# Optimization experiments

Hardware: AMD Instinct MI355X
Metric: run time of the kernel (lower is better)

The kernel has to match this reference:

```python
import jax, jax.numpy as jnp
import numpy as np

VOCAB, EMB, UNITS = 2000, 64, 512
B, T = 64, 128

def lstm(x_emb, Wx, Wh, b, h0, c0):
    """Keras LSTM: gates order (i, f, g, o), sigmoid recurrent activation, tanh activation.
    x_emb: [B, T, EMB]. Returns (H [B,T,U], h [B,U], c [B,U])."""
    # Precompute input contribution for all timesteps (one big GEMM)
    xz = jnp.einsum('bte,eu->btu', x_emb, Wx) + b  # [B, T, 4U]

    def step(carry, xz_t):
        h, c = carry
        z = xz_t + h @ Wh  # [B, 4U]
        i, f, g, o = jnp.split(z, 4, axis=-1)
        i = jax.nn.sigmoid(i)
        f = jax.nn.sigmoid(f)
        g = jnp.tanh(g)
        o = jax.nn.sigmoid(o)
        c = f * c + i * g
        h = o * jnp.tanh(c)
        return (h, c), h

    (h, c), H = jax.lax.scan(step, (h0, c0), jnp.swapaxes(xz, 0, 1))
    return jnp.swapaxes(H, 0, 1), h, c


def setup_inputs() -> dict:
    key = jax.random.key(0)
    ks = jax.random.split(key, 10)
    s = 0.05
    return {
        'x': jax.random.randint(ks[0], (B, T), 0, VOCAB),
        'y': jax.random.randint(ks[1], (B, T), 0, VOCAB),
        'enc_emb': jax.random.normal(ks[2], (VOCAB, EMB), jnp.float32) * s,
        'enc_Wx': jax.random.normal(ks[3], (EMB, 4 * UNITS), jnp.float32) * s,
        'enc_Wh': jax.random.normal(ks[4], (UNITS, 4 * UNITS), jnp.float32) * s,
        'enc_b': jnp.zeros((4 * UNITS,), jnp.float32),
        'dec_emb': jax.random.normal(ks[5], (VOCAB, EMB), jnp.float32) * s,
        'dec_Wx': jax.random.normal(ks[6], (EMB, 4 * UNITS), jnp.float32) * s,
        'dec_Wh': jax.random.normal(ks[7], (UNITS, 4 * UNITS), jnp.float32) * s,
        'dec_b': jnp.zeros((4 * UNITS,), jnp.float32),
        'dense_W': jax.random.normal(ks[8], (2 * UNITS, VOCAB), jnp.float32) * s,
        'dense_b': jnp.zeros((VOCAB,), jnp.float32),
    }


def reference(x, y, enc_emb, enc_Wx, enc_Wh, enc_b,
              dec_emb, dec_Wx, dec_Wh, dec_b, dense_W, dense_b):
    z0 = jnp.zeros((x.shape[0], UNITS), jnp.float32)
    # Encoder
    H, h, c = lstm(enc_emb[x], enc_Wx, enc_Wh, enc_b, z0, z0)  # H: [B,T,U]
    # Decoder LSTM
    s0 = h
    S, h2, c2 = lstm(dec_emb[y], dec_Wx, dec_Wh, dec_b, h, c)  # S: [B,T,U]
    # Shifted states as attention queries (teacher forcing, Luong dot-attention)
    S_ = jnp.concatenate([s0[:, None, :], S[:, :-1, :]], axis=1)  # [B,T,U]
    scores = jnp.einsum('bqu,bku->bqk', S_, H)  # [B,T,T]
    A = jnp.einsum('bqk,bku->bqu', jax.nn.softmax(scores, axis=-1), H)
    yo = jnp.concatenate([S, A], axis=-1)  # [B,T,2U]
    return jax.nn.softmax(yo @ dense_W + dense_b, axis=-1)  # [B,T,VOCAB]
```

## Files before the change

### kernel.cpp

```cpp
#include <hip/hip_runtime.h>
#include <math.h>

#define NB 64
#define NT 128
#define NE 64
#define NU 512
#define NG 2048
#define NV 2000
#define BU (NB*NU)
#define GRID_LSTM 256
#define KTOT 576
#define HS 584
#define WSTRIDE 584
#define SMEM_BYTES (64*WSTRIDE*2 + 16*HS*2 + 2*8*64*4)

#define ASSC 129
#define APB  136
#define OFF_SSC 0
#define OFF_PB  66048
#define OFF_ASM 100864
#define OFF_BSM 111104
#define SMEM_ATT 121344

typedef __attribute__((ext_vector_type(8))) short bf16x8;
typedef __attribute__((ext_vector_type(4))) float f32x4;
typedef __attribute__((ext_vector_type(8))) unsigned short u16x8;

__device__ __forceinline__ unsigned short f2bf(float x) {
    unsigned int u = __float_as_uint(x);
    u += 0x7FFFu + ((u >> 16) & 1u);
    return (unsigned short)(u >> 16);
}
__device__ __forceinline__ float fsigmoid(float x) {
    return __builtin_amdgcn_rcpf(1.f + __expf(-x));
}
__device__ __forceinline__ float ftanh(float x) {
    return 1.f - 2.f * __builtin_amdgcn_rcpf(__expf(2.f * x) + 1.f);
}

__global__ __launch_bounds__(512, 1)
void lstm2_coop(const int* __restrict__ xids, const int* __restrict__ yids,
                const unsigned short* __restrict__ embb_e,
                const unsigned short* __restrict__ embb_d,
                const unsigned short* __restrict__ WhT_e,
                const unsigned short* __restrict__ WhT_d,
                const float* __restrict__ enc_b, const float* __restrict__ dec_b,
                float* __restrict__ Hbuf, float* __restrict__ Sbuf,
                float* __restrict__ hping, float* __restrict__ hfin,
                unsigned short* __restrict__ yo,
                unsigned int* __restrict__ flags)
{
    extern __shared__ char smem[];
    unsigned short* whb  = (unsigned short*)smem;
    unsigned short* hlds = (unsigned short*)(smem + 64 * WSTRIDE * 2);
    float* zbuf = (float*)(smem + 64 * WSTRIDE * 2 + 16 * HS * 2);

    const int tid  = threadIdx.x;
    const int wv   = tid >> 6;
    const int cl   = tid & 63;
    const int bk   = blockIdx.x;
    const int rg   = bk & 7;
    const int cgi  = bk >> 3;
    const int brow0 = rg * 8;
    const int u0    = cgi * 16;

    const int bl  = tid >> 4;
    const int uug = tid & 15;
    float creg = 0.f;
    float b4[4] = {0.f, 0.f, 0.f, 0.f};
    if (tid < 128) {
#pragma unroll
        for (int g = 0; g < 4; ++g) b4[g] = enc_b[g * 512 + u0 + uug];
    }

    {
        const int cp = tid >> 3, ch = tid & 7;
        const int cg = (cp >> 4) * 512 + u0 + (cp & 15);
        const uint4* src = reinterpret_cast<const uint4*>(WhT_e + (size_t)cg * KTOT + ch * 72);
        uint4* dst = reinterpret_cast<uint4*>(whb + cp * WSTRIDE + ch * 72);
#pragma unroll
        for (int i = 0; i < 9; ++i) dst[i] = src[i];
    }

    const int col = wv * 64 + cl;
#pragma unroll
    for (int b = 0; b < 8; ++b) hlds[b * HS + col] = 0;
    for (int i = tid; i < 8 * HS; i += 512) hlds[8 * HS + i] = 0;
    {
        const int idb = xids[(brow0 + wv) * NT + 0];
        hlds[wv * HS + 512 + cl] = embb_e[(size_t)idb * NE + cl];
    }
    unsigned int* fl = flags + rg * 64;

    for (int T = 0; T < 2 * NT; ++T) {
        const int t = T & (NT - 1);
        float* Ho = (T < NT) ? Hbuf : Sbuf;
        __syncthreads();

        {
            const int g = wv & 3, half = wv >> 2;
            const int rr = cl & 15, kh = cl >> 4;
            f32x4 acc = {0.f, 0.f, 0.f, 0.f};
            const unsigned short* arow = hlds + rr * HS;
            const unsigned short* brow = whb + (g * 16 + rr) * WSTRIDE;
#pragma unroll
            for (int kt = 0; kt < 9; ++kt) {
                const int kb = (half * 9 + kt) * 32 + kh * 8;
                bf16x8 af = *reinterpret_cast<const bf16x8*>(arow + kb);
                bf16x8 bf = *reinterpret_cast<const bf16x8*>(brow + kb);
                acc = __builtin_amdgcn_mfma_f32_16x16x32_bf16(af, bf, acc, 0, 0, 0);
            }
            if (cl < 32) {
#pragma unroll
                for (int reg = 0; reg < 4; ++reg)
                    zbuf[half * 512 + (kh * 4 + reg) * 64 + g * 16 + rr] = acc[reg];
            }
        }
        __syncthreads();

        float h_ = 0.f;
        if (tid < 128) {
            float z[4];
#pragma unroll
            for (int g = 0; g < 4; ++g)
                z[g] = b4[g] + zbuf[bl * 64 + g * 16 + uug]
                             + zbuf[512 + bl * 64 + g * 16 + uug];
            const float i_ = fsigmoid(z[0]);
            const float f_ = fsigmoid(z[1]);
            const float g_ = ftanh(z[2]);
            const float o_ = fsigmoid(z[3]);
            creg = f_ * creg + i_ * g_;
            h_ = o_ * ftanh(creg);
            float* hw = hping + ((T + 1) & 1) * BU;
            __hip_atomic_store(&hw[(brow0 + bl) * NU + u0 + uug], h_,
                               __ATOMIC_RELAXED, __HIP_MEMORY_SCOPE_AGENT);
        }
        if (T == 2 * NT - 1) {
            if (tid < 128) {
                const size_t r = (size_t)(brow0 + bl) * NT + t;
                Ho[r * NU + u0 + uug] = h_;
                yo[r * 1024 + u0 + uug] = f2bf(h_);
            }
            break;
        }

        if (tid < 128)
            asm volatile("s_waitcnt vmcnt(0)" ::: "memory");
        __syncthreads();

        if (tid < 128 && (tid & 63) == 0)
            __hip_atomic_store(&fl[(tid >> 6) * 32 + cgi], (unsigned)(T + 1),
                               __ATOMIC_RELAXED, __HIP_MEMORY_SCOPE_AGENT);
        if (tid < 128) {
            const size_t r = (size_t)(brow0 + bl) * NT + t;
            Ho[r * NU + u0 + uug] = h_;
            if (T >= NT) yo[r * 1024 + u0 + uug] = f2bf(h_);
            if (T == NT - 1)
                hfin[(brow0 + bl) * NU + u0 + uug] = h_;
        }

        {
            const int Tn = T + 1;
            const int* nids = (Tn < NT) ? xids : yids;
            const unsigned short* nemb = (Tn < NT) ? embb_e : embb_d;
            const int idb = nids[(brow0 + wv) * NT + (Tn & (NT - 1))];
            hlds[wv * HS + 512 + cl] = nemb[(size_t)idb * NE + cl];
        }

        if (wv == 0) {
            const unsigned target = (unsigned)(T + 1);
            while (true) {
                unsigned v = __hip_atomic_load(&fl[cl], __ATOMIC_RELAXED,
                                               __HIP_MEMORY_SCOPE_AGENT);
#pragma unroll
                for (int o = 16; o; o >>= 1) {
                    unsigned v2 = (unsigned)__shfl_xor((int)v, o);
                    v = v2 < v ? v2 : v;
                }
                if (v >= target) break;
                __builtin_amdgcn_s_sleep(1);
            }
        }
        __syncthreads();

        {
            const float* hr = hping + ((T + 1) & 1) * BU + (size_t)brow0 * NU;
            float tmp[8];
#pragma unroll
            for (int b = 0; b < 8; ++b)
                tmp[b] = __hip_atomic_load(const_cast<float*>(&hr[b * NU + col]),
                                           __ATOMIC_RELAXED, __HIP_MEMORY_SCOPE_AGENT);
#pragma unroll
            for (int b = 0; b < 8; ++b) hlds[b * HS + col] = f2bf(tmp[b]);
        }

        if (T == NT - 1) {
            const int cp = tid >> 3, ch = tid & 7;
            const int cg = (cp >> 4) * 512 + u0 + (cp & 15);
            const uint4* src = reinterpret_cast<const uint4*>(WhT_d + (size_t)cg * KTOT + ch * 72);
            uint4* dst = reinterpret_cast<uint4*>(whb + cp * WSTRIDE + ch * 72);
#pragma unroll
            for (int i = 0; i < 9; ++i) dst[i] = src[i];
            if (tid < 128) {
#pragma unroll
                for (int g = 0; g < 4; ++g) b4[g] = dec_b[g * 512 + u0 + uug];
            }
        }
    }
}

__global__ __launch_bounds__(256)
void attn_mfma(const float* __restrict__ S, const float* __restrict__ Hbuf,
               const float* __restrict__ s0, unsigned short* __restrict__ yo)
{
    extern __shared__ char smem[];
    float* Ssc = (float*)(smem + OFF_SSC);
    unsigned short* Bc  = (unsigned short*)(smem + OFF_SSC);
    unsigned short* Pb  = (unsigned short*)(smem + OFF_PB);
    unsigned short* Asm_ = (unsigned short*)(smem + OFF_ASM);
    unsigned short* Bsm_ = (unsigned short*)(smem + OFF_BSM);

    const int tid  = threadIdx.x;
    const int wave = tid >> 6, lane = tid & 63;
    const int wm = wave >> 1, wn = wave & 1;
    const int rr = lane & 15, kh = lane >> 4;
    const int b = blockIdx.x;
    const float* Hb = Hbuf + (size_t)b * NT * NU;

    f32x4 acc[4][4];
#pragma unroll
    for (int m = 0; m < 4; ++m)
#pragma unroll
        for (int n = 0; n < 4; ++n) acc[m][n] = (f32x4){0.f, 0.f, 0.f, 0.f};

    for (int k0 = 0; k0 < 512; k0 += 32) {
        __syncthreads();
#pragma unroll
        for (int h = 0; h < 2; ++h) {
            const int row = (tid >> 2) + h * 64, seg = tid & 3;
            const float* qsrc = (row == 0) ? (s0 + (size_t)b * NU)
                                           : (S + ((size_t)b * NT + row - 1) * NU);
            const float4 a0 = reinterpret_cast<const float4*>(qsrc + k0 + seg * 8)[0];
            const float4 a1 = reinterpret_cast<const float4*>(qsrc + k0 + seg * 8)[1];
            u16x8 av;
            av[0] = f2bf(a0.x); av[1] = f2bf(a0.y); av[2] = f2bf(a0.z); av[3] = f2bf(a0.w);
            av[4] = f2bf(a1.x); av[5] = f2bf(a1.y); av[6] = f2bf(a1.z); av[7] = f2bf(a1.w);
            *reinterpret_cast<u16x8*>(Asm_ + row * 40 + seg * 8) = av;
            const float4 b0 = reinterpret_cast<const float4*>(Hb + (size_t)row * NU + k0 + seg * 8)[0];
            const float4 b1 = reinterpret_cast<const float4*>(Hb + (size_t)row * NU + k0 + seg * 8)[1];
            u16x8 bv;
            bv[0] = f2bf(b0.x); bv[1] = f2bf(b0.y); bv[2] = f2bf(b0.z); bv[3] = f2bf(b0.w);
            bv[4] = f2bf(b1.x); bv[5] = f2bf(b1.y); bv[6] = f2bf(b1.z); bv[7] = f2bf(b1.w);
            *reinterpret_cast<u16x8*>(Bsm_ + row * 40 + seg * 8) = bv;
        }
        __syncthreads();
        bf16x8 af[4], bfr[4];
#pragma unroll
        for (int m = 0; m < 4; ++m)
            af[m] = *reinterpret_cast<const bf16x8*>(Asm_ + (wm * 64 + m * 16 + rr) * 40 + kh * 8);
#pragma unroll
        for (int n = 0; n < 4; ++n)
            bfr[n] = *reinterpret_cast<const bf16x8*>(Bsm_ + (wn * 64 + n * 16 + rr) * 40 + kh * 8);
#pragma unroll
        for (int m = 0; m < 4; ++m)
#pragma unroll
            for (int n = 0; n < 4; ++n)
                acc[m][n] = __builtin_amdgcn_mfma_f32_16x16x32_bf16(af[m], bfr[n], acc[m][n], 0, 0, 0);
    }
    __syncthreads();
#pragma unroll
    for (int m = 0; m < 4; ++m)
#pragma unroll
        for (int n = 0; n < 4; ++n)
#pragma unroll
            for (int reg = 0; reg < 4; ++reg)
                Ssc[(wm * 64 + m * 16 + kh * 4 + reg) * ASSC + wn * 64 + n * 16 + rr] = acc[m][n][reg];
    __syncthreads();

    {
        const int row = tid >> 1, half = tid & 1;
        float* srow = Ssc + row * ASSC + half * 64;
        float mx = -INFINITY;
#pragma unroll 8
        for (int j = 0; j < 64; ++j) mx = fmaxf(mx, srow[j]);
        mx = fmaxf(mx, __shfl_xor(mx, 1));
        float sum = 0.f;
#pragma unroll 8
        for (int j = 0; j < 64; ++j) { float e = __expf(srow[j] - mx); srow[j] = e; sum += e; }
        sum += __shfl_xor(sum, 1);
        const float inv = 1.f / sum;
#pragma unroll 8
        for (int j = 0; j < 64; ++j)
            Pb[row * APB + half * 64 + j] = f2bf(srow[j] * inv);
    }

    for (int nc = 0; nc < 4; ++nc) {
        const int uc0 = nc * 128;
        __syncthreads();
#pragma unroll
        for (int c4 = 0; c4 < 4; ++c4) {
            const int kk = (tid >> 3) + 32 * c4;
            const int u0t = (tid & 7) * 16;
            const float* hsrc = Hb + (size_t)kk * NU + uc0 + u0t;
#pragma unroll
            for (int q4 = 0; q4 < 4; ++q4) {
                const float4 v = reinterpret_cast<const float4*>(hsrc)[q4];
                Bc[(u0t + q4 * 4 + 0) * APB + kk] = f2bf(v.x);
                Bc[(u0t + q4 * 4 + 1) * APB + kk] = f2bf(v.y);
                Bc[(u0t + q4 * 4 + 2) * APB + kk] = f2bf(v.z);
                Bc[(u0t + q4 * 4 + 3) * APB + kk] = f2bf(v.w);
            }
        }
        __syncthreads();

        f32x4 oacc[4][4];
#pragma unroll
        for (int m = 0; m < 4; ++m)
#pragma unroll
            for (int n = 0; n < 4; ++n) oacc[m][n] = (f32x4){0.f, 0.f, 0.f, 0.f};
#pragma unroll
        for (int ks = 0; ks < 4; ++ks) {
            bf16x8 af[4], bfr[4];
#pragma unroll
            for (int m = 0; m < 4; ++m)
                af[m] = *reinterpret_cast<const bf16x8*>(Pb + (wm * 64 + m * 16 + rr) * APB + ks * 32 + kh * 8);
#pragma unroll
            for (int n = 0; n < 4; ++n)
                bfr[n] = *reinterpret_cast<const bf16x8*>(Bc + (wn * 64 + n * 16 + rr) * APB + ks * 32 + kh * 8);
#pragma unroll
            for (int m = 0; m < 4; ++m)
#pragma unroll
                for (int n = 0; n < 4; ++n)
                    oacc[m][n] = __builtin_amdgcn_mfma_f32_16x16x32_bf16(af[m], bfr[n], oacc[m][n], 0, 0, 0);
        }
#pragma unroll
        for (int m = 0; m < 4; ++m)
#pragma unroll
            for (int n = 0; n < 4; ++n) {
                const int u = uc0 + wn * 64 + n * 16 + rr;
#pragma unroll
                for (int reg = 0; reg < 4; ++reg) {
                    const int q = wm * 64 + m * 16 + kh * 4 + reg;
                    yo[((size_t)b * NT + q) * 1024 + 512 + u] = f2bf(oacc[m][n][reg]);
                }
            }
    }
}

__global__ __launch_bounds__(256)
void conv_emb2(const float* __restrict__ e0, const float* __restrict__ e1,
               unsigned short* __restrict__ o0, unsigned short* __restrict__ o1,
               int n, int nbh)
{
    int b = blockIdx.x;
    const float* e = e0; unsigned short* o = o0;
    if (b >= nbh) { b -= nbh; e = e1; o = o1; }
    const int i = (b * 256 + threadIdx.x) * 8;
    if (i >= n) return;
    const float4 v0 = reinterpret_cast<const float4*>(e + i)[0];
    const float4 v1 = reinterpret_cast<const float4*>(e + i)[1];
    u16x8 r;
    r[0] = f2bf(v0.x); r[1] = f2bf(v0.y); r[2] = f2bf(v0.z); r[3] = f2bf(v0.w);
    r[4] = f2bf(v1.x); r[5] = f2bf(v1.y); r[6] = f2bf(v1.z); r[7] = f2bf(v1.w);
    *reinterpret_cast<u16x8*>(o + i) = r;
}

__global__ __launch_bounds__(256)
void conv_WhT2(const float* __restrict__ Wh_e, const float* __restrict__ Wx_e,
               const float* __restrict__ Wh_d, const float* __restrict__ Wx_d,
               unsigned short* __restrict__ WhT_e, unsigned short* __restrict__ WhT_d)
{
    __shared__ float lt[64][65];
    const float* Wh = (blockIdx.z == 0) ? Wh_e : Wh_d;
    const float* Wx = (blockIdx.z == 0) ? Wx_e : Wx_d;
    unsigned short* WhT = (blockIdx.z == 0) ? WhT_e : WhT_d;
    const int tid = threadIdx.x;
    const int c0 = blockIdx.x * 64;
    const int k0 = blockIdx.y * 64;
#pragma unroll
    for (int j = 0; j < 16; ++j) {
        const int lin = tid + 256 * j;
        const int kk = lin >> 6, cc = lin & 63;
        const int k = k0 + kk;
        lt[cc][kk] = (k < 512) ? Wh[(size_t)k * NG + c0 + cc]
                               : Wx[(size_t)(k - 512) * NG + c0 + cc];
    }
    __syncthreads();
    const int c = tid >> 2, kseg = tid & 3;
    unsigned short tmp[16];
#pragma unroll
    for (int m = 0; m < 16; ++m)
        tmp[m] = f2bf(lt[c][kseg * 16 + m]);
    unsigned short* dst = WhT + (size_t)(c0 + c) * KTOT + k0 + kseg * 16;
    *reinterpret_cast<u16x8*>(dst)     = *reinterpret_cast<u16x8*>(tmp);
    *reinterpret_cast<u16x8*>(dst + 8) = *reinterpret_cast<u16x8*>(tmp + 8);
}

__global__ __launch_bounds__(256)
void conv_Wt(const float* __restrict__ W, unsigned short* __restrict__ Wt)
{
    __shared__ float lt[64][65];
    const int tid = threadIdx.x;
    const int c0 = blockIdx.x * 64;
    const int k0 = blockIdx.y * 64;
#pragma unroll
    for (int j = 0; j < 16; ++j) {
        const int lin = tid + 256 * j;
        const int kk = lin >> 6, cc = lin & 63;
        const int c = c0 + cc;
        lt[cc][kk] = (c < NV) ? W[(size_t)(k0 + kk) * NV + c] : 0.f;
    }
    __syncthreads();
    const int c = tid >> 2, kseg = tid & 3;
    unsigned short tmp[16];
#pragma unroll
    for (int m = 0; m < 16; ++m)
        tmp[m] = f2bf(lt[c][kseg * 16 + m]);
    unsigned short* dst = Wt + (size_t)(c0 + c) * 1024 + k0 + kseg * 16;
    *reinterpret_cast<u16x8*>(dst)     = *reinterpret_cast<u16x8*>(tmp);
    *reinterpret_cast<u16x8*>(dst + 8) = *reinterpret_cast<u16x8*>(tmp + 8);
}

__global__ __launch_bounds__(256)
void dense_mfma(const unsigned short* __restrict__ yo,
                const unsigned short* __restrict__ Wt,
                const float* __restrict__ bias, float* __restrict__ out)
{
    __shared__ unsigned short Asm[128][40];
    __shared__ unsigned short Bsm[128][40];
    const int tid  = threadIdx.x;
    const int wave = tid >> 6, lane = tid & 63;
    const int wm = wave >> 1, wn = wave & 1;
    const int r0 = blockIdx.y * 128, c0 = blockIdx.x * 128;
    const int rr = lane & 15, kh = lane >> 4;

    f32x4 acc[4][4];
#pragma unroll
    for (int m = 0; m < 4; ++m)
#pragma unroll
        for (int n = 0; n < 4; ++n) acc[m][n] = (f32x4){0.f, 0.f, 0.f, 0.f};

    for (int k0 = 0; k0 < 1024; k0 += 32) {
        __syncthreads();
#pragma unroll
        for (int h = 0; h < 2; ++h) {
            const int row = (tid >> 2) + h * 64, seg = tid & 3;
            *reinterpret_cast<uint4*>(&Asm[row][seg * 8]) =
                *reinterpret_cast<const uint4*>(yo + (size_t)(r0 + row) * 1024 + k0 + seg * 8);
            *reinterpret_cast<uint4*>(&Bsm[row][seg * 8]) =
                *reinterpret_cast<const uint4*>(Wt + (size_t)(c0 + row) * 1024 + k0 + seg * 8);
        }
        __syncthreads();
        bf16x8 af[4], bfr[4];
#pragma unroll
        for (int m = 0; m < 4; ++m)
            af[m] = *reinterpret_cast<const bf16x8*>(&Asm[wm * 64 + m * 16 + rr][kh * 8]);
#pragma unroll
        for (int n = 0; n < 4; ++n)
            bfr[n] = *reinterpret_cast<const bf16x8*>(&Bsm[wn * 64 + n * 16 + rr][kh * 8]);
#pragma unroll
        for (int m = 0; m < 4; ++m)
#pragma unroll
            for (int n = 0; n < 4; ++n)
                acc[m][n] = __builtin_amdgcn_mfma_f32_16x16x32_bf16(af[m], bfr[n], acc[m][n], 0, 0, 0);
    }

#pragma unroll
    for (int m = 0; m < 4; ++m) {
#pragma unroll
        for (int n = 0; n < 4; ++n) {
            const int c = c0 + wn * 64 + n * 16 + rr;
            if (c < NV) {
                const float bc = bias[c];
#pragma unroll
                for (int reg = 0; reg < 4; ++reg) {
                    const int r = r0 + wm * 64 + m * 16 + kh * 4 + reg;
                    out[(size_t)r * NV + c] = acc[m][n][reg] + bc;
                }
            }
        }
    }
}

__global__ __launch_bounds__(256)
void softmax_rows(float* __restrict__ out)
{
    __shared__ float red[4];
    const int t = threadIdx.x;
    float* row = out + (size_t)blockIdx.x * NV;

    float v[8];
    float m = -INFINITY;
#pragma unroll
    for (int i = 0; i < 8; ++i) {
        const int j = t + 256 * i;
        v[i] = (j < NV) ? row[j] : -INFINITY;
        m = fmaxf(m, v[i]);
    }
#pragma unroll
    for (int o = 32; o; o >>= 1) m = fmaxf(m, __shfl_xor(m, o));
    if ((t & 63) == 0) red[t >> 6] = m;
    __syncthreads();
    m = fmaxf(fmaxf(red[0], red[1]), fmaxf(red[2], red[3]));
    __syncthreads();

    float s = 0.f;
#pragma unroll
    for (int i = 0; i < 8; ++i) {
        const int j = t + 256 * i;
        if (j < NV) { v[i] = expf(v[i] - m); s += v[i]; }
    }
#pragma unroll
    for (int o = 32; o; o >>= 1) s += __shfl_xor(s, o);
    if ((t & 63) == 0) red[t >> 6] = s;
    __syncthreads();
    const float inv = 1.f / (red[0] + red[1] + red[2] + red[3]);
#pragma unroll
    for (int i = 0; i < 8; ++i) {
        const int j = t + 256 * i;
        if (j < NV) row[j] = v[i] * inv;
    }
}

extern "C" void kernel_launch(void* const* d_in, const int* in_sizes, int n_in,
                              void* d_out, int out_size, void* d_ws, size_t ws_size,
                              hipStream_t stream)
{
    const int*   x       = (const int*)  d_in[0];
    const int*   y       = (const int*)  d_in[1];
    const float* enc_emb = (const float*)d_in[2];
    const float* enc_Wx  = (const float*)d_in[3];
    const float* enc_Wh  = (const float*)d_in[4];
    const float* enc_b   = (const float*)d_in[5];
    const float* dec_emb = (const float*)d_in[6];
    const float* dec_Wx  = (const float*)d_in[7];
    const float* dec_Wh  = (const float*)d_in[8];
    const float* dec_b   = (const float*)d_in[9];
    const float* dns_W   = (const float*)d_in[10];
    const float* dns_b   = (const float*)d_in[11];
    float* out = (float*)d_out;

    float* ws   = (float*)d_ws;
    float* Hbuf = ws;
    float* Sbuf = Hbuf + (size_t)NB * NT * NU;
    unsigned short* yo = (unsigned short*)(Sbuf + (size_t)NB * NT * NU);
    unsigned short* Wt = yo + (size_t)NB * NT * 1024;
    float* hping = (float*)(Wt + (size_t)2048 * 1024);
    float* hfin  = hping + 2 * BU;
    unsigned int* bar0 = (unsigned int*)(hfin + BU);
    unsigned short* WhT_e = (unsigned short*)(bar0 + 512);
    unsigned short* WhT_d = WhT_e + (size_t)2048 * KTOT;
    unsigned short* embb_e = WhT_d + (size_t)2048 * KTOT;
    unsigned short* embb_d = embb_e + (size_t)NV * NE;

    hipMemsetAsync(bar0, 0, 512 * sizeof(unsigned int), stream);

    (void)hipFuncSetAttribute(reinterpret_cast<const void*>(lstm2_coop),
                              hipFuncAttributeMaxDynamicSharedMemorySize, SMEM_BYTES);
    (void)hipFuncSetAttribute(reinterpret_cast<const void*>(attn_mfma),
                              hipFuncAttributeMaxDynamicSharedMemorySize, SMEM_ATT);

    const int nemb = NV * NE, nbh = (nemb / 8 + 255) / 256;
    conv_emb2<<<dim3(2 * nbh), dim3(256), 0, stream>>>(enc_emb, dec_emb, embb_e, embb_d, nemb, nbh);
    conv_WhT2<<<dim3(32, 9, 2), dim3(256), 0, stream>>>(enc_Wh, enc_Wx, dec_Wh, dec_Wx, WhT_e, WhT_d);
    conv_Wt<<<dim3(32, 16), dim3(256), 0, stream>>>(dns_W, Wt);

    {
        void* args[] = { (void*)&x, (void*)&y, (void*)&embb_e, (void*)&embb_d,
                         (void*)&WhT_e, (void*)&WhT_d, (void*)&enc_b, (void*)&dec_b,
                         (void*)&Hbuf, (void*)&Sbuf, (void*)&hping, (void*)&hfin,
                         (void*)&yo, (void*)&bar0 };
        (void)hipLaunchCooperativeKernel(reinterpret_cast<void*>(lstm2_coop),
                                         dim3(GRID_LSTM), dim3(512), args,
                                         SMEM_BYTES, stream);
    }
    attn_mfma<<<dim3(NB), dim3(256), SMEM_ATT, stream>>>(Sbuf, Hbuf, hfin, yo);
    dense_mfma<<<dim3(16, 64), dim3(256), 0, stream>>>(yo, Wt, dns_b, out);
    softmax_rows<<<dim3(NB * NT), dim3(256), 0, stream>>>(out);
}
```

Measured before the change: 880.7 us.

## Split attention blocks by query half and merge weight conversion kernels

The attention kernel now launches two blocks per batch, each handling 64 query rows, so 128 blocks run instead of 64 and the shared memory footprint shrinks. Each block still loads and converts the full key matrix H, which doubles that work across the grid. The three weight and embedding conversion kernels are merged into one launch to save launch overhead. The softmax stage now runs on only half of the threads.

```diff
diff --git a/kernel.cpp b/kernel.cpp
--- a/kernel.cpp
+++ b/kernel.cpp
@@ -17,10 +17,10 @@
 #define ASSC 129
 #define APB  136
 #define OFF_SSC 0
-#define OFF_PB  66048
-#define OFF_ASM 100864
-#define OFF_BSM 111104
-#define SMEM_ATT 121344
+#define OFF_PB  34816
+#define OFF_ASM 52224
+#define OFF_BSM 57344
+#define SMEM_ATT 67584
 
 typedef __attribute__((ext_vector_type(8))) short bf16x8;
 typedef __attribute__((ext_vector_type(4))) float f32x4;
@@ -224,28 +224,33 @@
     const int wave = tid >> 6, lane = tid & 63;
     const int wm = wave >> 1, wn = wave & 1;
     const int rr = lane & 15, kh = lane >> 4;
-    const int b = blockIdx.x;
+    const int b  = blockIdx.x >> 1;
+    const int qh = blockIdx.x & 1;
     const float* Hb = Hbuf + (size_t)b * NT * NU;
 
-    f32x4 acc[4][4];
-#pragma unroll
-    for (int m = 0; m < 4; ++m)
+    f32x4 acc[2][4];
+#pragma unroll
+    for (int m = 0; m < 2; ++m)
 #pragma unroll
         for (int n = 0; n < 4; ++n) acc[m][n] = (f32x4){0.f, 0.f, 0.f, 0.f};
 
     for (int k0 = 0; k0 < 512; k0 += 32) {
         __syncthreads();
-#pragma unroll
-        for (int h = 0; h < 2; ++h) {
-            const int row = (tid >> 2) + h * 64, seg = tid & 3;
-            const float* qsrc = (row == 0) ? (s0 + (size_t)b * NU)
-                                           : (S + ((size_t)b * NT + row - 1) * NU);
+        {
+            const int row = tid >> 2, seg = tid & 3;
+            const int q = qh * 64 + row;
+            const float* qsrc = (q == 0) ? (s0 + (size_t)b * NU)
+                                         : (S + ((size_t)b * NT + q - 1) * NU);
             const float4 a0 = reinterpret_cast<const float4*>(qsrc + k0 + seg * 8)[0];
             const float4 a1 = reinterpret_cast<const float4*>(qsrc + k0 + seg * 8)[1];
             u16x8 av;
             av[0] = f2bf(a0.x); av[1] = f2bf(a0.y); av[2] = f2bf(a0.z); av[3] = f2bf(a0.w);
             av[4] = f2bf(a1.x); av[5] = f2bf(a1.y); av[6] = f2bf(a1.z); av[7] = f2bf(a1.w);
             *reinterpret_cast<u16x8*>(Asm_ + row * 40 + seg * 8) = av;
+        }
+#pragma unroll
+        for (int h = 0; h < 2; ++h) {
+            const int row = (tid >> 2) + h * 64, seg = tid & 3;
             const float4 b0 = reinterpret_cast<const float4*>(Hb + (size_t)row * NU + k0 + seg * 8)[0];
             const float4 b1 = reinterpret_cast<const float4*>(Hb + (size_t)row * NU + k0 + seg * 8)[1];
             u16x8 bv;
@@ -254,30 +259,30 @@
             *reinterpret_cast<u16x8*>(Bsm_ + row * 40 + seg * 8) = bv;
         }
         __syncthreads();
-        bf16x8 af[4], bfr[4];
-#pragma unroll
-        for (int m = 0; m < 4; ++m)
-            af[m] = *reinterpret_cast<const bf16x8*>(Asm_ + (wm * 64 + m * 16 + rr) * 40 + kh * 8);
+        bf16x8 af[2], bfr[4];
+#pragma unroll
+        for (int m = 0; m < 2; ++m)
+            af[m] = *reinterpret_cast<const bf16x8*>(Asm_ + (wm * 32 + m * 16 + rr) * 40 + kh * 8);
 #pragma unroll
         for (int n = 0; n < 4; ++n)
             bfr[n] = *reinterpret_cast<const bf16x8*>(Bsm_ + (wn * 64 + n * 16 + rr) * 40 + kh * 8);
 #pragma unroll
-        for (int m = 0; m < 4; ++m)
+        for (int m = 0; m < 2; ++m)
 #pragma unroll
             for (int n = 0; n < 4; ++n)
                 acc[m][n] = __builtin_amdgcn_mfma_f32_16x16x32_bf16(af[m], bfr[n], acc[m][n], 0, 0, 0);
     }
     __syncthreads();
 #pragma unroll
-    for (int m = 0; m < 4; ++m)
+    for (int m = 0; m < 2; ++m)
 #pragma unroll
         for (int n = 0; n < 4; ++n)
 #pragma unroll
             for (int reg = 0; reg < 4; ++reg)
-                Ssc[(wm * 64 + m * 16 + kh * 4 + reg) * ASSC + wn * 64 + n * 16 + rr] = acc[m][n][reg];
+                Ssc[(wm * 32 + m * 16 + kh * 4 + reg) * ASSC + wn * 64 + n * 16 + rr] = acc[m][n][reg];
     __syncthreads();
 
-    {
+    if (tid < 128) {
         const int row = tid >> 1, half = tid & 1;
         float* srow = Ssc + row * ASSC + half * 64;
         float mx = -INFINITY;
@@ -313,34 +318,34 @@
         }
         __syncthreads();
 
-        f32x4 oacc[4][4];
-#pragma unroll
-        for (int m = 0; m < 4; ++m)
+        f32x4 oacc[2][4];
+#pragma unroll
+        for (int m = 0; m < 2; ++m)
 #pragma unroll
             for (int n = 0; n < 4; ++n) oacc[m][n] = (f32x4){0.f, 0.f, 0.f, 0.f};
 #pragma unroll
         for (int ks = 0; ks < 4; ++ks) {
-            bf16x8 af[4], bfr[4];
-#pragma unroll
-            for (int m = 0; m < 4; ++m)
-                af[m] = *reinterpret_cast<const bf16x8*>(Pb + (wm * 64 + m * 16 + rr) * APB + ks * 32 + kh * 8);
+            bf16x8 af[2], bfr[4];
+#pragma unroll
+            for (int m = 0; m < 2; ++m)
+                af[m] = *reinterpret_cast<const bf16x8*>(Pb + (wm * 32 + m * 16 + rr) * APB + ks * 32 + kh * 8);
 #pragma unroll
             for (int n = 0; n < 4; ++n)
                 bfr[n] = *reinterpret_cast<const bf16x8*>(Bc + (wn * 64 + n * 16 + rr) * APB + ks * 32 + kh * 8);
 #pragma unroll
-            for (int m = 0; m < 4; ++m)
+            for (int m = 0; m < 2; ++m)
 #pragma unroll
                 for (int n = 0; n < 4; ++n)
                     oacc[m][n] = __builtin_amdgcn_mfma_f32_16x16x32_bf16(af[m], bfr[n], oacc[m][n], 0, 0, 0);
         }
 #pragma unroll
-        for (int m = 0; m < 4; ++m)
+        for (int m = 0; m < 2; ++m)
 #pragma unroll
             for (int n = 0; n < 4; ++n) {
                 const int u = uc0 + wn * 64 + n * 16 + rr;
 #pragma unroll
                 for (int reg = 0; reg < 4; ++reg) {
-                    const int q = wm * 64 + m * 16 + kh * 4 + reg;
+                    const int q = qh * 64 + wm * 32 + m * 16 + kh * 4 + reg;
                     yo[((size_t)b * NT + q) * 1024 + 512 + u] = f2bf(oacc[m][n][reg]);
                 }
             }
@@ -348,77 +353,82 @@
 }
 
 __global__ __launch_bounds__(256)
-void conv_emb2(const float* __restrict__ e0, const float* __restrict__ e1,
-               unsigned short* __restrict__ o0, unsigned short* __restrict__ o1,
-               int n, int nbh)
-{
-    int b = blockIdx.x;
-    const float* e = e0; unsigned short* o = o0;
-    if (b >= nbh) { b -= nbh; e = e1; o = o1; }
-    const int i = (b * 256 + threadIdx.x) * 8;
-    if (i >= n) return;
-    const float4 v0 = reinterpret_cast<const float4*>(e + i)[0];
-    const float4 v1 = reinterpret_cast<const float4*>(e + i)[1];
-    u16x8 r;
-    r[0] = f2bf(v0.x); r[1] = f2bf(v0.y); r[2] = f2bf(v0.z); r[3] = f2bf(v0.w);
-    r[4] = f2bf(v1.x); r[5] = f2bf(v1.y); r[6] = f2bf(v1.z); r[7] = f2bf(v1.w);
-    *reinterpret_cast<u16x8*>(o + i) = r;
-}
-
-__global__ __launch_bounds__(256)
-void conv_WhT2(const float* __restrict__ Wh_e, const float* __restrict__ Wx_e,
-               const float* __restrict__ Wh_d, const float* __restrict__ Wx_d,
-               unsigned short* __restrict__ WhT_e, unsigned short* __restrict__ WhT_d)
-{
-    __shared__ float lt[64][65];
-    const float* Wh = (blockIdx.z == 0) ? Wh_e : Wh_d;
-    const float* Wx = (blockIdx.z == 0) ? Wx_e : Wx_d;
-    unsigned short* WhT = (blockIdx.z == 0) ? WhT_e : WhT_d;
-    const int tid = threadIdx.x;
-    const int c0 = blockIdx.x * 64;
-    const int k0 = blockIdx.y * 64;
-#pragma unroll
-    for (int j = 0; j < 16; ++j) {
-        const int lin = tid + 256 * j;
-        const int kk = lin >> 6, cc = lin & 63;
-        const int k = k0 + kk;
-        lt[cc][kk] = (k < 512) ? Wh[(size_t)k * NG + c0 + cc]
-                               : Wx[(size_t)(k - 512) * NG + c0 + cc];
-    }
-    __syncthreads();
-    const int c = tid >> 2, kseg = tid & 3;
-    unsigned short tmp[16];
-#pragma unroll
-    for (int m = 0; m < 16; ++m)
-        tmp[m] = f2bf(lt[c][kseg * 16 + m]);
-    unsigned short* dst = WhT + (size_t)(c0 + c) * KTOT + k0 + kseg * 16;
-    *reinterpret_cast<u16x8*>(dst)     = *reinterpret_cast<u16x8*>(tmp);
-    *reinterpret_cast<u16x8*>(dst + 8) = *reinterpret_cast<u16x8*>(tmp + 8);
-}
-
-__global__ __launch_bounds__(256)
-void conv_Wt(const float* __restrict__ W, unsigned short* __restrict__ Wt)
+void conv_all(const float* __restrict__ enc_emb, const float* __restrict__ dec_emb,
+              const float* __restrict__ Wh_e, const float* __restrict__ Wx_e,
+              const float* __restrict__ Wh_d, const float* __restrict__ Wx_d,
+              const float* __restrict__ dns_W,
+              unsigned short* __restrict__ embb_e, unsigned short* __restrict__ embb_d,
+              unsigned short* __restrict__ WhT_e, unsigned short* __restrict__ WhT_d,
+              unsigned short* __restrict__ Wt, int nbh)
 {
     __shared__ float lt[64][65];
     const int tid = threadIdx.x;
-    const int c0 = blockIdx.x * 64;
-    const int k0 = blockIdx.y * 64;
-#pragma unroll
-    for (int j = 0; j < 16; ++j) {
-        const int lin = tid + 256 * j;
-        const int kk = lin >> 6, cc = lin & 63;
-        const int c = c0 + cc;
-        lt[cc][kk] = (c < NV) ? W[(size_t)(k0 + kk) * NV + c] : 0.f;
-    }
-    __syncthreads();
-    const int c = tid >> 2, kseg = tid & 3;
-    unsigned short tmp[16];
-#pragma unroll
-    for (int m = 0; m < 16; ++m)
-        tmp[m] = f2bf(lt[c][kseg * 16 + m]);
-    unsigned short* dst = Wt + (size_t)(c0 + c) * 1024 + k0 + kseg * 16;
-    *reinterpret_cast<u16x8*>(dst)     = *reinterpret_cast<u16x8*>(tmp);
-    *reinterpret_cast<u16x8*>(dst + 8) = *reinterpret_cast<u16x8*>(tmp + 8);
+    int blk = blockIdx.x;
+
+    if (blk < 2 * nbh) {
+        const float* e = (blk < nbh) ? enc_emb : dec_emb;
+        unsigned short* o = (blk < nbh) ? embb_e : embb_d;
+        const int bb = (blk < nbh) ? blk : blk - nbh;
+        const int i = (bb * 256 + tid) * 8;
+        if (i < NV * NE) {
+            const float4 v0 = reinterpret_cast<const float4*>(e + i)[0];
+            const float4 v1 = reinterpret_cast<const float4*>(e + i)[1];
+            u16x8 r;
+            r[0] = f2bf(v0.x); r[1] = f2bf(v0.y); r[2] = f2bf(v0.z); r[3] = f2bf(v0.w);
+            r[4] = f2bf(v1.x); r[5] = f2bf(v1.y); r[6] = f2bf(v1.z); r[7] = f2bf(v1.w);
+            *reinterpret_cast<u16x8*>(o + i) = r;
+        }
+        return;
+    }
+    blk -= 2 * nbh;
+
+    if (blk < 576) {
+        const int z  = blk / 288;
+        const int rem = blk - z * 288;
+        const int ky = rem >> 5, cx = rem & 31;
+        const float* Wh = z ? Wh_d : Wh_e;
+        const float* Wx = z ? Wx_d : Wx_e;
+        unsigned short* WhT = z ? WhT_d : WhT_e;
+        const int c0 = cx * 64, k0 = ky * 64;
+#pragma unroll
+        for (int j = 0; j < 16; ++j) {
+            const int lin = tid + 256 * j;
+            const int kk = lin >> 6, cc = lin & 63;
+            const int k = k0 + kk;
+            lt[cc][kk] = (k < 512) ? Wh[(size_t)k * NG + c0 + cc]
+                                   : Wx[(size_t)(k - 512) * NG + c0 + cc];
+        }
+        __syncthreads();
+        const int c = tid >> 2, kseg = tid & 3;
+        unsigned short tmp[16];
+#pragma unroll
+        for (int m = 0; m < 16; ++m) tmp[m] = f2bf(lt[c][kseg * 16 + m]);
+        unsigned short* dst = WhT + (size_t)(c0 + c) * KTOT + k0 + kseg * 16;
+        *reinterpret_cast<u16x8*>(dst)     = *reinterpret_cast<u16x8*>(tmp);
+        *reinterpret_cast<u16x8*>(dst + 8) = *reinterpret_cast<u16x8*>(tmp + 8);
+        return;
+    }
+    blk -= 576;
+
+    {
+        const int ky = blk >> 5, cx = blk & 31;
+        const int c0 = cx * 64, k0 = ky * 64;
+#pragma unroll
+        for (int j = 0; j < 16; ++j) {
+            const int lin = tid + 256 * j;
+            const int kk = lin >> 6, cc = lin & 63;
+            const int c = c0 + cc;
+            lt[cc][kk] = (c < NV) ? dns_W[(size_t)(k0 + kk) * NV + c] : 0.f;
+        }
+        __syncthreads();
+        const int c = tid >> 2, kseg = tid & 3;
+        unsigned short tmp[16];
+#pragma unroll
+        for (int m = 0; m < 16; ++m) tmp[m] = f2bf(lt[c][kseg * 16 + m]);
+        unsigned short* dst = Wt + (size_t)(c0 + c) * 1024 + k0 + kseg * 16;
+        *reinterpret_cast<u16x8*>(dst)     = *reinterpret_cast<u16x8*>(tmp);
+        *reinterpret_cast<u16x8*>(dst + 8) = *reinterpret_cast<u16x8*>(tmp + 8);
+    }
 }
 
 __global__ __launch_bounds__(256)
@@ -561,9 +571,9 @@
                               hipFuncAttributeMaxDynamicSharedMemorySize, SMEM_ATT);
 
     const int nemb = NV * NE, nbh = (nemb / 8 + 255) / 256;
-    conv_emb2<<<dim3(2 * nbh), dim3(256), 0, stream>>>(enc_emb, dec_emb, embb_e, embb_d, nemb, nbh);
-    conv_WhT2<<<dim3(32, 9, 2), dim3(256), 0, stream>>>(enc_Wh, enc_Wx, dec_Wh, dec_Wx, WhT_e, WhT_d);
-    conv_Wt<<<dim3(32, 16), dim3(256), 0, stream>>>(dns_W, Wt);
+    conv_all<<<dim3(2 * nbh + 576 + 512), dim3(256), 0, stream>>>(
+        enc_emb, dec_emb, enc_Wh, enc_Wx, dec_Wh, dec_Wx, dns_W,
+        embb_e, embb_d, WhT_e, WhT_d, Wt, nbh);
 
     {
         void* args[] = { (void*)&x, (void*)&y, (void*)&embb_e, (void*)&embb_d,
@@ -574,7 +584,7 @@
                                          dim3(GRID_LSTM), dim3(512), args,
                                          SMEM_BYTES, stream);
     }
-    attn_mfma<<<dim3(NB), dim3(256), SMEM_ATT, stream>>>(Sbuf, Hbuf, hfin, yo);
+    attn_mfma<<<dim3(NB * 2), dim3(256), SMEM_ATT, stream>>>(Sbuf, Hbuf, hfin, yo);
     dense_mfma<<<dim3(16, 64), dim3(256), 0, stream>>>(yo, Wt, dns_b, out);
     softmax_rows<<<dim3(NB * NT), dim3(256), 0, stream>>>(out);
 }
```

Result: no change. 863.9 us (-1.9%).
